# Optimization experiments

Hardware: AMD Instinct MI355X
Metric: run time of the kernel (lower is better)

The kernel has to match this reference:

```python
import jax, jax.numpy as jnp
import numpy as np

EMBED_DIM = 1024
NUM_HEADS = 16
HEAD_DIM = EMBED_DIM // NUM_HEADS
SEQ_LEN = 2048
BATCH = 2
THETA_BASE = 10000.0


def rope_angles(head_dim, max_seq_len):
    inv_freq = 1.0 / (THETA_BASE ** (jnp.arange(0, head_dim, 2, dtype=jnp.float32) / head_dim))
    pos = jnp.arange(max_seq_len, dtype=jnp.float32)
    angles = pos[:, None] * inv_freq[None, :]              # [S, D/2]
    angles = jnp.concatenate([angles, angles], axis=-1)    # [S, D]
    return jnp.cos(angles), jnp.sin(angles)


def apply_rope(x, cos, sin):
    # x: [B, H, S, D]; cos/sin: [S, D]
    d = x.shape[-1]
    x1, x2 = x[..., : d // 2], x[..., d // 2 :]
    rotated = jnp.concatenate([-x2, x1], axis=-1)
    return x * cos[None, None, :, :] + rotated * sin[None, None, :, :]


def setup_inputs() -> dict:
    key = jax.random.key(0)
    kx, kq, kk, kv, ko = jax.random.split(key, 5)
    s = 1.0 / np.sqrt(EMBED_DIM)
    return {
        "x": jax.random.normal(kx, (BATCH, SEQ_LEN, EMBED_DIM), dtype=jnp.float32),
        "Wq": jax.random.normal(kq, (EMBED_DIM, EMBED_DIM), dtype=jnp.float32) * s,
        "Wk": jax.random.normal(kk, (EMBED_DIM, EMBED_DIM), dtype=jnp.float32) * s,
        "Wv": jax.random.normal(kv, (EMBED_DIM, EMBED_DIM), dtype=jnp.float32) * s,
        "Wo": jax.random.normal(ko, (EMBED_DIM, EMBED_DIM), dtype=jnp.float32) * s,
    }


def reference(x, Wq, Wk, Wv, Wo):
    B, S, E = x.shape
    H, D = NUM_HEADS, HEAD_DIM
    cos, sin = rope_angles(D, S)

    def split_heads(t):
        return t.reshape(B, S, H, D).transpose(0, 2, 1, 3)  # [B,H,S,D]

    q = split_heads(x @ Wq.T)
    k = split_heads(x @ Wk.T)
    v = split_heads(x @ Wv.T)

    q = apply_rope(q, cos, sin)
    k = apply_rope(k, cos, sin)

    scores = jnp.einsum("bhsd,bhtd->bhst", q, k)
    causal = jnp.triu(jnp.ones((S, S), dtype=bool), k=1)
    scores = jnp.where(causal[None, None, :, :], -jnp.inf, scores)
    weights = jax.nn.softmax(scores / jnp.sqrt(jnp.float32(D)), axis=-1)

    ctx = jnp.einsum("bhst,bhtd->bhsd", weights, v)
    ctx = ctx.transpose(0, 2, 1, 3).reshape(B, S, E)
    return ctx @ Wo.T
```

## Files before the change

kernel.cpp:

```cpp
#include <hip/hip_runtime.h>
#include <hip/hip_bf16.h>

#define H_NUM 16
#define D_DIM 64
#define S_LEN 2048
#define EMB   1024
#define M_TOT 4096

typedef unsigned short u16;
typedef unsigned int   u32;
typedef __attribute__((ext_vector_type(8))) short short8;
typedef __attribute__((ext_vector_type(4))) float f32x4;

__device__ __forceinline__ u32 f2bf_u(float f) {
    u32 u = __float_as_uint(f);
    return (u + 0x7fffu + ((u >> 16) & 1u)) >> 16;
}
__device__ __forceinline__ u32 pack2(float a, float b) {
    return f2bf_u(a) | (f2bf_u(b) << 16);
}
__device__ __forceinline__ u32 pack2t(float a, float b) {
    return __builtin_amdgcn_perm(__float_as_uint(b), __float_as_uint(a),
                                 0x07060302u);
}
__device__ __forceinline__ uint4 pack8(float4 lo, float4 hi) {
    return make_uint4(pack2(lo.x, lo.y), pack2(lo.z, lo.w),
                      pack2(hi.x, hi.y), pack2(hi.z, hi.w));
}

__device__ __forceinline__ void lds_dma16(const u16* g, u16* l) {
    __builtin_amdgcn_global_load_lds(
        (const __attribute__((address_space(1))) void*)g,
        (__attribute__((address_space(3))) void*)l, 16, 0, 0);
}

__global__ __launch_bounds__(256) void cast_kernel(
    const float* __restrict__ x,  const float* __restrict__ Wq,
    const float* __restrict__ Wk, const float* __restrict__ Wv,
    const float* __restrict__ Wo, u16* __restrict__ ws, float2* __restrict__ tab)
{
    const int seg = blockIdx.y;
    if (seg == 5) {
        const int idx = blockIdx.x * 256 + threadIdx.x;
        if (idx < S_LEN * 32) {
            const int s = idx >> 5, d = idx & 31;
            const float ang = (float)s * __expf(-(float)d * 0.28782313662425573f);
            tab[idx] = make_float2(cosf(ang), sinf(ang));
        }
        return;
    }
    const float* src = (seg == 0) ? x : (seg == 1) ? Wq : (seg == 2) ? Wk
                     : (seg == 3) ? Wv : Wo;
    u16* dst = (seg == 0) ? ws : ws + (3 + seg) * 1048576;
    const int n = (seg == 0) ? 4194304 : 1048576;
    const int idx = (blockIdx.x * 256 + threadIdx.x) * 8;
    if (idx < n) {
        float4 lo = *(const float4*)(src + idx);
        float4 hi = *(const float4*)(src + idx + 4);
        *(uint4*)(dst + idx) = pack8(lo, hi);
    }
}

__global__ __launch_bounds__(256) void qkv_rope_kernel(
    const u16* __restrict__ xb, const u16* __restrict__ wb,
    const float2* __restrict__ tab,
    u16* __restrict__ qo, u16* __restrict__ ko, u16* __restrict__ vo)
{
    const int w  = blockIdx.y >> 3;
    const int nb = blockIdx.y & 7;
    const u16* W = wb + w * 1048576;

    __shared__ __align__(16) u16 smem[12288];
    u16* As = smem;
    u16* Bs = smem + 64 * 64;
    u16 (*Ep)[132] = (u16(*)[132])smem;

    const int tid   = threadIdx.x;
    const int lane  = tid & 63;
    const int wid   = tid >> 6;
    const int waveM = wid >> 1;
    const int waveN = wid & 1;
    const int col16 = lane & 15;
    const int quad  = lane >> 4;

    const int m0 = blockIdx.x * 64;
    const int n0 = nb * 128;

    f32x4 acc[2][4];
    const f32x4 zero4 = {0.f, 0.f, 0.f, 0.f};
#pragma unroll
    for (int i = 0; i < 2; i++)
#pragma unroll
        for (int j = 0; j < 4; j++) acc[i][j] = zero4;

    const int drow = tid >> 3;
    const int dpos = tid & 7;
    const u16* Ag = xb + (size_t)m0 * EMB;
    const u16* Bg = W  + (size_t)n0 * EMB;

    for (int k0 = 0; k0 < EMB; k0 += 64) {
        __syncthreads();
#pragma unroll
        for (int j = 0; j < 2; j++) {
            const int rl = j * 32 + drow;
            const int cg = dpos ^ (rl & 7);
            lds_dma16(Ag + (size_t)rl * EMB + k0 + cg * 8,
                      As + (j * 32 + wid * 8) * 64);
        }
#pragma unroll
        for (int j = 0; j < 4; j++) {
            const int rl = j * 32 + drow;
            const int cg = dpos ^ (rl & 7);
            lds_dma16(Bg + (size_t)rl * EMB + k0 + cg * 8,
                      Bs + (j * 32 + wid * 8) * 64);
        }
        __syncthreads();

        short8 af[2][2], bf[4][2];
#pragma unroll
        for (int mt = 0; mt < 2; mt++) {
            const int r = waveM * 32 + mt * 16 + col16;
#pragma unroll
            for (int ks = 0; ks < 2; ks++) {
                const int p = (ks * 4 + quad) ^ (r & 7);
                af[mt][ks] = *(const short8*)(As + r * 64 + p * 8);
            }
        }
#pragma unroll
        for (int nt = 0; nt < 4; nt++) {
            const int r = waveN * 64 + nt * 16 + col16;
#pragma unroll
            for (int ks = 0; ks < 2; ks++) {
                const int p = (ks * 4 + quad) ^ (r & 7);
                bf[nt][ks] = *(const short8*)(Bs + r * 64 + p * 8);
            }
        }
#pragma unroll
        for (int ks = 0; ks < 2; ks++)
#pragma unroll
            for (int mt = 0; mt < 2; mt++)
#pragma unroll
                for (int nt = 0; nt < 4; nt++)
                    acc[mt][nt] = __builtin_amdgcn_mfma_f32_16x16x32_bf16(
                        af[mt][ks], bf[nt][ks], acc[mt][nt], 0, 0, 0);
    }

    const float qs = (w == 0) ? 0.18033688011112042f : 1.0f;
    __syncthreads();
#pragma unroll
    for (int mt = 0; mt < 2; mt++) {
#pragma unroll
        for (int r = 0; r < 4; r++) {
            const int m_local = waveM * 32 + mt * 16 + quad * 4 + r;
            const int s = (m0 + m_local) & 2047;
            if (w == 2) {
#pragma unroll
                for (int nt = 0; nt < 4; nt++)
                    Ep[m_local][waveN * 64 + nt * 16 + col16] =
                        (u16)f2bf_u(acc[mt][nt][r]);
            } else {
#pragma unroll
                for (int nt = 0; nt < 2; nt++) {
                    const int d = nt * 16 + col16;
                    const float2 cs = tab[s * 32 + d];
                    const float lo = acc[mt][nt][r];
                    const float hi = acc[mt][nt + 2][r];
                    Ep[m_local][waveN * 64 + d]      =
                        (u16)f2bf_u((lo * cs.x - hi * cs.y) * qs);
                    Ep[m_local][waveN * 64 + d + 32] =
                        (u16)f2bf_u((hi * cs.x + lo * cs.y) * qs);
                }
            }
        }
    }
    __syncthreads();

    const int b = m0 >> 11;
    if (w != 2) {
        u16* out = (w == 0) ? qo : ko;
#pragma unroll
        for (int j = 0; j < 4; j++) {
            const int g = j * 256 + tid;
            const int head_local = g >> 9;
            const int sl  = (g >> 3) & 63;
            const int cir = g & 7;
            uint4 val = *(const uint4*)(&Ep[sl][head_local * 64 + cir * 8]);
            const int h = (n0 >> 6) + head_local;
            const size_t base = (((size_t)(b * H_NUM + h)) * S_LEN + (m0 & 2047)) * 64;
            *(uint4*)(out + base + (size_t)(g & 511) * 8) = val;
        }
    } else {
        const int s0 = m0 & 2047;
#pragma unroll
        for (int j = 0; j < 4; j++) {
            const int g = j * 256 + tid;
            const int d_all = g >> 3;
            const int sc = g & 7;
            u32 wv[4];
#pragma unroll
            for (int hw = 0; hw < 4; hw++) {
                const int p0 = sc * 8 + hw * 2;
                const int r0 = ((p0 & 3) << 4) | (p0 >> 2);
                const int p1 = p0 + 1;
                const int r1 = ((p1 & 3) << 4) | (p1 >> 2);
                wv[hw] = (u32)Ep[r0][d_all] | ((u32)Ep[r1][d_all] << 16);
            }
            const int h = (n0 >> 6) + (d_all >> 6);
            const int d = d_all & 63;
            *(uint4*)(vo + ((size_t)(b * H_NUM + h) * 64 + d) * 2048 + s0 + sc * 8) =
                make_uint4(wv[0], wv[1], wv[2], wv[3]);
        }
    }
}

__global__ __launch_bounds__(512) void attn_kernel(
    const u16* __restrict__ q, const u16* __restrict__ k,
    const u16* __restrict__ v, u16* __restrict__ ctx)
{
    __shared__ __align__(16) u16 QPA[64 * 64];
    __shared__ __align__(16) u16 QPB[64 * 64];
    __shared__ __align__(16) u16 Ks[2][64 * 64];
    __shared__ __align__(16) u16 VTs[2][64 * 64];

    const int tid   = threadIdx.x;
    const int lane  = tid & 63;
    const int wid   = tid >> 6;
    const int w4    = wid & 3;
    const bool isB  = (wid >= 4);
    const int col16 = lane & 15;
    const int quad  = lane >> 4;

    const int bh = blockIdx.x;
    const int p  = blockIdx.y;
    const int qbA = p;
    const int qbB = 31 - p;
    const int myQb   = isB ? qbB : qbA;
    const int myBase = myQb * 64;
    const size_t bhOff = (size_t)bh * S_LEN * D_DIM;

    const int srow = tid >> 3;
    const int spos = tid & 7;
    const int scg  = spos ^ (srow & 7);

    u16* qdst = isB ? QPB : QPA;

    auto stage = [&](int kt, int buf) {
        lds_dma16(k + bhOff + (size_t)(kt * 64 + srow) * 64 + scg * 8,
                  &Ks[buf][wid * 512]);
        lds_dma16(v + bhOff + (size_t)srow * 2048 + kt * 64 + scg * 8,
                  &VTs[buf][wid * 512]);
    };

    stage(0, 0);
    {
        const int r5 = srow & 31;
#pragma unroll
        for (int j = 0; j < 2; j++) {
            const int rl = j * 32 + r5;
            const int cg = spos ^ (rl & 7);
            lds_dma16(q + bhOff + (size_t)(myBase + rl) * 64 + cg * 8,
                      qdst + (j * 32 + w4 * 8) * 64);
        }
    }
    __syncthreads();

    short8 qf[2];
    {
        const int rq = w4 * 16 + col16;
#pragma unroll
        for (int ks = 0; ks < 2; ks++) {
            const int c = (ks * 4 + quad) ^ (rq & 7);
            qf[ks] = *(const short8*)(qdst + rq * 64 + c * 8);
        }
    }

    const short ONE = (short)0x3F80;
    const short8 onesf = {ONE, ONE, ONE, ONE, ONE, ONE, ONE, ONE};

    f32x4 O[4];
    const f32x4 zero4 = {0.f, 0.f, 0.f, 0.f};
#pragma unroll
    for (int j = 0; j < 4; j++) O[j] = zero4;
    f32x4 lacc = zero4;

    for (int kt = 0; kt <= qbB; kt++) {
        if (kt > 0) __syncthreads();
        if (kt < qbB) stage(kt + 1, (kt + 1) & 1);
        const int cur = kt & 1;

        if (kt > myQb) continue;

        f32x4 sc[4];
#pragma unroll
        for (int nt = 0; nt < 4; nt++) sc[nt] = zero4;
#pragma unroll
        for (int ks = 0; ks < 2; ks++) {
            short8 kf[4];
#pragma unroll
            for (int nt = 0; nt < 4; nt++) {
                const int rk = nt * 16 + col16;
                const int c = (ks * 4 + quad) ^ (rk & 7);
                kf[nt] = *(const short8*)(&Ks[cur][rk * 64 + c * 8]);
            }
            __builtin_amdgcn_s_setprio(1);
#pragma unroll
            for (int nt = 0; nt < 4; nt++)
                sc[nt] = __builtin_amdgcn_mfma_f32_16x16x32_bf16(
                    qf[ks], kf[nt], sc[nt], 0, 0, 0);
            __builtin_amdgcn_s_setprio(0);
        }

        if (kt == myQb) {
#pragma unroll
            for (int r = 0; r < 4; r++) {
                const int qg = myBase + w4 * 16 + quad * 4 + r;
#pragma unroll
                for (int nt = 0; nt < 4; nt++) {
                    const int kg = kt * 64 + nt * 16 + col16;
                    float pv = __builtin_amdgcn_exp2f(sc[nt][r]);
                    if (kg > qg) pv = 0.f;
                    sc[nt][r] = pv;
                }
            }
        } else {
#pragma unroll
            for (int r = 0; r < 4; r++)
#pragma unroll
                for (int nt = 0; nt < 4; nt++)
                    sc[nt][r] = __builtin_amdgcn_exp2f(sc[nt][r]);
        }

#pragma unroll
        for (int r = 0; r < 4; r++) {
            const int ml = quad * 4 + r;
            const u32 lo = pack2t(sc[0][r], sc[1][r]);
            const u32 hi = pack2t(sc[2][r], sc[3][r]);
            *(uint2*)(qdst + (w4 * 16 + ml) * 64 +
                      (((col16 >> 1) ^ (ml & 7)) * 8 + (col16 & 1) * 4)) =
                make_uint2(lo, hi);
        }

#pragma unroll
        for (int ks = 0; ks < 2; ks++) {
            short8 pf, vf[4];
            {
                const int c = (ks * 4 + quad) ^ (col16 & 7);
                pf = *(const short8*)(qdst + (w4 * 16 + col16) * 64 + c * 8);
            }
#pragma unroll
            for (int dt = 0; dt < 4; dt++) {
                const int d = dt * 16 + col16;
                const int c = (ks * 4 + quad) ^ (d & 7);
                vf[dt] = *(const short8*)(&VTs[cur][d * 64 + c * 8]);
            }
            __builtin_amdgcn_s_setprio(1);
#pragma unroll
            for (int dt = 0; dt < 4; dt++)
                O[dt] = __builtin_amdgcn_mfma_f32_16x16x32_bf16(
                    pf, vf[dt], O[dt], 0, 0, 0);
            lacc = __builtin_amdgcn_mfma_f32_16x16x32_bf16(
                pf, onesf, lacc, 0, 0, 0);
            __builtin_amdgcn_s_setprio(0);
        }
    }

    const int b = bh >> 4, h = bh & 15;
#pragma unroll
    for (int r = 0; r < 4; r++) {
        const int ml = quad * 4 + r;
        const float inv = __builtin_amdgcn_rcpf(lacc[r]);
        const u32 lo = pack2t(O[0][r] * inv, O[1][r] * inv);
        const u32 hi = pack2t(O[2][r] * inv, O[3][r] * inv);
        *(uint2*)(qdst + (w4 * 16 + ml) * 64 +
                  (((col16 >> 1) ^ (ml & 7)) * 8 + (col16 & 1) * 4)) =
            make_uint2(lo, hi);
    }
#pragma unroll
    for (int j = 0; j < 2; j++) {
        const int gg  = j * 64 + lane;
        const int sl = gg >> 3;
        const int cir = gg & 7;
        u32 wv[4];
#pragma unroll
        for (int hw = 0; hw < 4; hw++) {
            const int d0 = cir * 8 + hw * 2;
            const int p0 = ((d0 & 15) << 2) | (d0 >> 4);
            const int d1 = d0 + 1;
            const int p1 = ((d1 & 15) << 2) | (d1 >> 4);
            const u16 v0 = qdst[(w4 * 16 + sl) * 64 + ((p0 >> 3) ^ (sl & 7)) * 8 + (p0 & 7)];
            const u16 v1 = qdst[(w4 * 16 + sl) * 64 + ((p1 >> 3) ^ (sl & 7)) * 8 + (p1 & 7)];
            wv[hw] = (u32)v0 | ((u32)v1 << 16);
        }
        const size_t rowbase =
            ((size_t)b * S_LEN + myBase + w4 * 16 + sl) * EMB + h * 64;
        *(uint4*)(ctx + rowbase + cir * 8) = make_uint4(wv[0], wv[1], wv[2], wv[3]);
    }
}

__global__ __launch_bounds__(256) void proj_kernel(
    const u16* __restrict__ X, const u16* __restrict__ W, float* __restrict__ out)
{
    __shared__ __align__(16) u16 smem[8192];
    u16* As = smem;
    u16* Bs = smem + 64 * 64;

    const int tid   = threadIdx.x;
    const int lane  = tid & 63;
    const int wid   = tid >> 6;
    const int col16 = lane & 15;
    const int quad  = lane >> 4;

    const int m0 = blockIdx.x * 64;
    const int n0 = blockIdx.y * 64;

    f32x4 acc[4];
    const f32x4 zero4 = {0.f, 0.f, 0.f, 0.f};
#pragma unroll
    for (int i = 0; i < 4; i++) acc[i] = zero4;

    const int drow = tid >> 3;
    const int dpos = tid & 7;
    const u16* Ag = X + (size_t)m0 * EMB;
    const u16* Bg = W + (size_t)n0 * EMB;

    for (int k0 = 0; k0 < EMB; k0 += 64) {
        __syncthreads();
#pragma unroll
        for (int j = 0; j < 2; j++) {
            const int rl = j * 32 + drow;
            const int cg = dpos ^ (rl & 7);
            lds_dma16(Ag + (size_t)rl * EMB + k0 + cg * 8,
                      As + (j * 32 + wid * 8) * 64);
        }
#pragma unroll
        for (int j = 0; j < 2; j++) {
            const int rl = j * 32 + drow;
            const int cg = dpos ^ (rl & 7);
            lds_dma16(Bg + (size_t)rl * EMB + k0 + cg * 8,
                      Bs + (j * 32 + wid * 8) * 64);
        }
        __syncthreads();

        short8 af[2], bf[4][2];
        {
            const int r = wid * 16 + col16;
#pragma unroll
            for (int ks = 0; ks < 2; ks++) {
                const int p = (ks * 4 + quad) ^ (r & 7);
                af[ks] = *(const short8*)(As + r * 64 + p * 8);
            }
        }
#pragma unroll
        for (int nt = 0; nt < 4; nt++) {
            const int r = nt * 16 + col16;
#pragma unroll
            for (int ks = 0; ks < 2; ks++) {
                const int p = (ks * 4 + quad) ^ (r & 7);
                bf[nt][ks] = *(const short8*)(Bs + r * 64 + p * 8);
            }
        }
#pragma unroll
        for (int ks = 0; ks < 2; ks++)
#pragma unroll
            for (int nt = 0; nt < 4; nt++)
                acc[nt] = __builtin_amdgcn_mfma_f32_16x16x32_bf16(
                    bf[nt][ks], af[ks], acc[nt], 0, 0, 0);
    }

#pragma unroll
    for (int nt = 0; nt < 4; nt++) {
        const int m_g = m0 + wid * 16 + col16;
        const int n_g = n0 + nt * 16 + quad * 4;
        *(f32x4*)(out + (size_t)m_g * EMB + n_g) = acc[nt];
    }
}

extern "C" void kernel_launch(void* const* d_in, const int* in_sizes, int n_in,
                              void* d_out, int out_size, void* d_ws, size_t ws_size,
                              hipStream_t stream)
{
    const float* x  = (const float*)d_in[0];
    const float* Wq = (const float*)d_in[1];
    const float* Wk = (const float*)d_in[2];
    const float* Wv = (const float*)d_in[3];
    const float* Wo = (const float*)d_in[4];

    u16* ws = (u16*)d_ws;
    u16* xb  = ws;
    u16* wb  = ws + 4194304;
    u16* wob = ws + 7340032;
    u16* q   = ws + 8388608;
    u16* k   = ws + 12582912;
    u16* v   = ws + 16777216;
    u16* ctx = ws + 20971520;
    float2* tab = (float2*)(ws + 25165824);

    cast_kernel<<<dim3(2048, 6), 256, 0, stream>>>(x, Wq, Wk, Wv, Wo, ws, tab);
    qkv_rope_kernel<<<dim3(64, 24), 256, 0, stream>>>(xb, wb, tab, q, k, v);
    attn_kernel<<<dim3(32, 16), 512, 0, stream>>>(q, k, v, ctx);
    proj_kernel<<<dim3(64, 16), 256, 0, stream>>>(ctx, wob, (float*)d_out);
}
```

Baseline: 164.3 us.

## Double-buffer LDS tiles in QKV and output projection GEMMs

```diff
diff --git a/kernel.cpp b/kernel.cpp
--- a/kernel.cpp
+++ b/kernel.cpp
@@ -70,9 +70,7 @@
     const int nb = blockIdx.y & 7;
     const u16* W = wb + w * 1048576;
 
-    __shared__ __align__(16) u16 smem[12288];
-    u16* As = smem;
-    u16* Bs = smem + 64 * 64;
+    __shared__ __align__(16) u16 smem[24576];
     u16 (*Ep)[132] = (u16(*)[132])smem;
 
     const int tid   = threadIdx.x;
@@ -98,8 +96,10 @@
     const u16* Ag = xb + (size_t)m0 * EMB;
     const u16* Bg = W  + (size_t)n0 * EMB;
 
-    for (int k0 = 0; k0 < EMB; k0 += 64) {
-        __syncthreads();
+    auto stage = [&](int kk, int buf) {
+        u16* As = smem + buf * 4096;
+        u16* Bs = smem + 8192 + buf * 8192;
+        const int k0 = kk * 64;
 #pragma unroll
         for (int j = 0; j < 2; j++) {
             const int rl = j * 32 + drow;
@@ -114,7 +114,16 @@
             lds_dma16(Bg + (size_t)rl * EMB + k0 + cg * 8,
                       Bs + (j * 32 + wid * 8) * 64);
         }
-        __syncthreads();
+    };
+
+    stage(0, 0);
+    __syncthreads();
+
+    for (int kk = 0; kk < 16; kk++) {
+        if (kk > 0) __syncthreads();
+        if (kk < 15) stage(kk + 1, (kk + 1) & 1);
+        const u16* As = smem + (kk & 1) * 4096;
+        const u16* Bs = smem + 8192 + (kk & 1) * 8192;
 
         short8 af[2][2], bf[4][2];
 #pragma unroll
@@ -400,9 +409,7 @@
 __global__ __launch_bounds__(256) void proj_kernel(
     const u16* __restrict__ X, const u16* __restrict__ W, float* __restrict__ out)
 {
-    __shared__ __align__(16) u16 smem[8192];
-    u16* As = smem;
-    u16* Bs = smem + 64 * 64;
+    __shared__ __align__(16) u16 smem[16384];
 
     const int tid   = threadIdx.x;
     const int lane  = tid & 63;
@@ -423,8 +430,10 @@
     const u16* Ag = X + (size_t)m0 * EMB;
     const u16* Bg = W + (size_t)n0 * EMB;
 
-    for (int k0 = 0; k0 < EMB; k0 += 64) {
-        __syncthreads();
+    auto stage = [&](int kk, int buf) {
+        u16* As = smem + buf * 4096;
+        u16* Bs = smem + 8192 + buf * 4096;
+        const int k0 = kk * 64;
 #pragma unroll
         for (int j = 0; j < 2; j++) {
             const int rl = j * 32 + drow;
@@ -439,7 +448,16 @@
             lds_dma16(Bg + (size_t)rl * EMB + k0 + cg * 8,
                       Bs + (j * 32 + wid * 8) * 64);
         }
-        __syncthreads();
+    };
+
+    stage(0, 0);
+    __syncthreads();
+
+    for (int kk = 0; kk < 16; kk++) {
+        if (kk > 0) __syncthreads();
+        if (kk < 15) stage(kk + 1, (kk + 1) & 1);
+        const u16* As = smem + (kk & 1) * 4096;
+        const u16* Bs = smem + 8192 + (kk & 1) * 4096;
 
         short8 af[2], bf[4][2];
         {
```

New measurement: 168.7 us. 1.03x slower.

## Process two K/V tiles per barrier with double-buffered paired staging

Applied to the files above, without the earlier changes.

```diff
diff --git a/kernel.cpp b/kernel.cpp
--- a/kernel.cpp
+++ b/kernel.cpp
@@ -219,8 +219,8 @@
 {
     __shared__ __align__(16) u16 QPA[64 * 64];
     __shared__ __align__(16) u16 QPB[64 * 64];
-    __shared__ __align__(16) u16 Ks[2][64 * 64];
-    __shared__ __align__(16) u16 VTs[2][64 * 64];
+    __shared__ __align__(16) u16 Ks[2][2][64 * 64];
+    __shared__ __align__(16) u16 VTs[2][2][64 * 64];
 
     const int tid   = threadIdx.x;
     const int lane  = tid & 63;
@@ -244,14 +244,15 @@
 
     u16* qdst = isB ? QPB : QPA;
 
-    auto stage = [&](int kt, int buf) {
+    auto stage = [&](int kt, int buf, int slot) {
         lds_dma16(k + bhOff + (size_t)(kt * 64 + srow) * 64 + scg * 8,
-                  &Ks[buf][wid * 512]);
+                  &Ks[buf][slot][wid * 512]);
         lds_dma16(v + bhOff + (size_t)srow * 2048 + kt * 64 + scg * 8,
-                  &VTs[buf][wid * 512]);
+                  &VTs[buf][slot][wid * 512]);
     };
 
-    stage(0, 0);
+    stage(0, 0, 0);
+    stage(1, 0, 1);
     {
         const int r5 = srow & 31;
 #pragma unroll
@@ -283,85 +284,93 @@
     for (int j = 0; j < 4; j++) O[j] = zero4;
     f32x4 lacc = zero4;
 
-    for (int kt = 0; kt <= qbB; kt++) {
-        if (kt > 0) __syncthreads();
-        if (kt < qbB) stage(kt + 1, (kt + 1) & 1);
-        const int cur = kt & 1;
-
-        if (kt > myQb) continue;
-
-        f32x4 sc[4];
-#pragma unroll
-        for (int nt = 0; nt < 4; nt++) sc[nt] = zero4;
-#pragma unroll
-        for (int ks = 0; ks < 2; ks++) {
-            short8 kf[4];
-#pragma unroll
-            for (int nt = 0; nt < 4; nt++) {
-                const int rk = nt * 16 + col16;
-                const int c = (ks * 4 + quad) ^ (rk & 7);
-                kf[nt] = *(const short8*)(&Ks[cur][rk * 64 + c * 8]);
-            }
-            __builtin_amdgcn_s_setprio(1);
-#pragma unroll
-            for (int nt = 0; nt < 4; nt++)
-                sc[nt] = __builtin_amdgcn_mfma_f32_16x16x32_bf16(
-                    qf[ks], kf[nt], sc[nt], 0, 0, 0);
-            __builtin_amdgcn_s_setprio(0);
-        }
-
-        if (kt == myQb) {
+    int buf = 0;
+    for (int kt0 = 0; kt0 <= qbB; kt0 += 2) {
+        if (kt0 > 0) __syncthreads();
+        if (kt0 + 2 <= qbB) {
+            stage(kt0 + 2, buf ^ 1, 0);
+            if (kt0 + 3 <= qbB) stage(kt0 + 3, buf ^ 1, 1);
+        }
+
+#pragma unroll
+        for (int sl = 0; sl < 2; sl++) {
+            const int kt = kt0 + sl;
+            if (kt > qbB || kt > myQb) continue;
+
+            f32x4 sc[4];
+#pragma unroll
+            for (int nt = 0; nt < 4; nt++) sc[nt] = zero4;
+#pragma unroll
+            for (int ks = 0; ks < 2; ks++) {
+                short8 kf[4];
+#pragma unroll
+                for (int nt = 0; nt < 4; nt++) {
+                    const int rk = nt * 16 + col16;
+                    const int c = (ks * 4 + quad) ^ (rk & 7);
+                    kf[nt] = *(const short8*)(&Ks[buf][sl][rk * 64 + c * 8]);
+                }
+                __builtin_amdgcn_s_setprio(1);
+#pragma unroll
+                for (int nt = 0; nt < 4; nt++)
+                    sc[nt] = __builtin_amdgcn_mfma_f32_16x16x32_bf16(
+                        qf[ks], kf[nt], sc[nt], 0, 0, 0);
+                __builtin_amdgcn_s_setprio(0);
+            }
+
+            if (kt == myQb) {
+#pragma unroll
+                for (int r = 0; r < 4; r++) {
+                    const int qg = myBase + w4 * 16 + quad * 4 + r;
+#pragma unroll
+                    for (int nt = 0; nt < 4; nt++) {
+                        const int kg = kt * 64 + nt * 16 + col16;
+                        float pv = __builtin_amdgcn_exp2f(sc[nt][r]);
+                        if (kg > qg) pv = 0.f;
+                        sc[nt][r] = pv;
+                    }
+                }
+            } else {
+#pragma unroll
+                for (int r = 0; r < 4; r++)
+#pragma unroll
+                    for (int nt = 0; nt < 4; nt++)
+                        sc[nt][r] = __builtin_amdgcn_exp2f(sc[nt][r]);
+            }
+
 #pragma unroll
             for (int r = 0; r < 4; r++) {
-                const int qg = myBase + w4 * 16 + quad * 4 + r;
-#pragma unroll
-                for (int nt = 0; nt < 4; nt++) {
-                    const int kg = kt * 64 + nt * 16 + col16;
-                    float pv = __builtin_amdgcn_exp2f(sc[nt][r]);
-                    if (kg > qg) pv = 0.f;
-                    sc[nt][r] = pv;
+                const int ml = quad * 4 + r;
+                const u32 lo = pack2t(sc[0][r], sc[1][r]);
+                const u32 hi = pack2t(sc[2][r], sc[3][r]);
+                *(uint2*)(qdst + (w4 * 16 + ml) * 64 +
+                          (((col16 >> 1) ^ (ml & 7)) * 8 + (col16 & 1) * 4)) =
+                    make_uint2(lo, hi);
+            }
+
+#pragma unroll
+            for (int ks = 0; ks < 2; ks++) {
+                short8 pf, vf[4];
+                {
+                    const int c = (ks * 4 + quad) ^ (col16 & 7);
+                    pf = *(const short8*)(qdst + (w4 * 16 + col16) * 64 + c * 8);
                 }
-            }
-        } else {
-#pragma unroll
-            for (int r = 0; r < 4; r++)
-#pragma unroll
-                for (int nt = 0; nt < 4; nt++)
-                    sc[nt][r] = __builtin_amdgcn_exp2f(sc[nt][r]);
-        }
-
-#pragma unroll
-        for (int r = 0; r < 4; r++) {
-            const int ml = quad * 4 + r;
-            const u32 lo = pack2t(sc[0][r], sc[1][r]);
-            const u32 hi = pack2t(sc[2][r], sc[3][r]);
-            *(uint2*)(qdst + (w4 * 16 + ml) * 64 +
-                      (((col16 >> 1) ^ (ml & 7)) * 8 + (col16 & 1) * 4)) =
-                make_uint2(lo, hi);
-        }
-
-#pragma unroll
-        for (int ks = 0; ks < 2; ks++) {
-            short8 pf, vf[4];
-            {
-                const int c = (ks * 4 + quad) ^ (col16 & 7);
-                pf = *(const short8*)(qdst + (w4 * 16 + col16) * 64 + c * 8);
-            }
-#pragma unroll
-            for (int dt = 0; dt < 4; dt++) {
-                const int d = dt * 16 + col16;
-                const int c = (ks * 4 + quad) ^ (d & 7);
-                vf[dt] = *(const short8*)(&VTs[cur][d * 64 + c * 8]);
-            }
-            __builtin_amdgcn_s_setprio(1);
-#pragma unroll
-            for (int dt = 0; dt < 4; dt++)
-                O[dt] = __builtin_amdgcn_mfma_f32_16x16x32_bf16(
-                    pf, vf[dt], O[dt], 0, 0, 0);
-            lacc = __builtin_amdgcn_mfma_f32_16x16x32_bf16(
-                pf, onesf, lacc, 0, 0, 0);
-            __builtin_amdgcn_s_setprio(0);
-        }
+#pragma unroll
+                for (int dt = 0; dt < 4; dt++) {
+                    const int d = dt * 16 + col16;
+                    const int c = (ks * 4 + quad) ^ (d & 7);
+                    vf[dt] = *(const short8*)(&VTs[buf][sl][d * 64 + c * 8]);
+                }
+                __builtin_amdgcn_s_setprio(1);
+#pragma unroll
+                for (int dt = 0; dt < 4; dt++)
+                    O[dt] = __builtin_amdgcn_mfma_f32_16x16x32_bf16(
+                        pf, vf[dt], O[dt], 0, 0, 0);
+                lacc = __builtin_amdgcn_mfma_f32_16x16x32_bf16(
+                    pf, onesf, lacc, 0, 0, 0);
+                __builtin_amdgcn_s_setprio(0);
+            }
+        }
+        buf ^= 1;
     }
 
     const int b = bh >> 4, h = bh & 15;
```

After: 161.1 us. -2.0%, faster.
